# Optimization experiments

Hardware: AMD Instinct MI355X
Metric: run time of the kernel (lower is better)

## Reference

```python
import jax, jax.numpy as jnp
import numpy as np

NUM_EDGE = 5
NUM_CHANNELS = 2
NUM_NODES = 2048
W_IN = 256
W_OUT = 128
NUM_CLASS = 16
NUM_LAYERS = 2


def gtconv(A, w):
    """Softmax-weighted mix of edge-type adjacencies.
    A: [E, N, N], w: [E, C] -> [C, N, N].
    Equivalent to concatenating COO edge lists scaled by filter[j, i] and
    summing duplicates (what the scipy round-trip does implicitly)."""
    f = jax.nn.softmax(w, axis=0)  # softmax over edge types (dim=0)
    return jnp.einsum('enm,ec->cnm', A, f)


def degree_normalize(H):
    """GTN.normalization: deg = scatter_add over col, value *= deg[col]^-1 (col scaling).
    H: [C, N, N]; deg over rows (axis=1) gives per-column in-degree."""
    deg = H.sum(axis=1)  # [C, N]
    dinv = jnp.where(deg > 0, 1.0 / jnp.where(deg > 0, deg, 1.0), 0.0)
    return H * dinv[:, None, :]


def setup_inputs() -> dict:
    key = jax.random.key(0)
    ks = jax.random.split(key, 8)
    A = jax.random.uniform(ks[0], (NUM_EDGE, NUM_NODES, NUM_NODES), dtype=jnp.float32)
    h = jax.random.normal(ks[1], (NUM_NODES, W_IN), dtype=jnp.float32)
    # GTConv weights: init std=0.01 as in reset_parameters
    w1 = jax.random.normal(ks[2], (NUM_EDGE, NUM_CHANNELS), dtype=jnp.float32) * 0.01
    w2 = jax.random.normal(ks[3], (NUM_EDGE, NUM_CHANNELS), dtype=jnp.float32) * 0.01
    w_layers = jax.random.normal(ks[4], (NUM_LAYERS - 1, NUM_EDGE, NUM_CHANNELS), dtype=jnp.float32) * 0.01
    gcn_w = jax.random.normal(ks[5], (W_IN, W_OUT), dtype=jnp.float32) * (1.0 / np.sqrt(W_IN))
    gcn_b = jnp.zeros((W_OUT,), dtype=jnp.float32)
    lin1_w = jax.random.normal(ks[6], (W_OUT * NUM_CHANNELS, W_OUT), dtype=jnp.float32) * (1.0 / np.sqrt(W_OUT * NUM_CHANNELS))
    lin1_b = jnp.zeros((W_OUT,), dtype=jnp.float32)
    lin2_w = jax.random.normal(ks[7], (W_OUT, NUM_CLASS), dtype=jnp.float32) * (1.0 / np.sqrt(W_OUT))
    lin2_b = jnp.zeros((NUM_CLASS,), dtype=jnp.float32)
    return {"A": A, "h": h, "w1": w1, "w2": w2, "w_layers": w_layers,
            "gcn_w": gcn_w, "gcn_b": gcn_b, "lin1_w": lin1_w, "lin1_b": lin1_b,
            "lin2_w": lin2_w, "lin2_b": lin2_b}


def reference(A, h, w1, w2, w_layers, gcn_w, gcn_b, lin1_w, lin1_b, lin2_w, lin2_b):
    # Layer 0 (first=True): H[c] = conv1(A)[c] @ conv2(A)[c], then degree norm.
    H = jnp.einsum('cnk,ckm->cnm', gtconv(A, w1), gtconv(A, w2))
    H = degree_normalize(H)
    # Layers 1..L-1 (first=False): H[c] = H[c] @ conv(A)[c], then degree norm.
    for i in range(w_layers.shape[0]):
        B = gtconv(A, w_layers[i])
        H = jnp.einsum('cnk,ckm->cnm', H, B)
        H = degree_normalize(H)
    # Shared GCN per channel (DGL GraphConv, norm='both'): weight first (w_in > w_out),
    # src out-degree^-1/2 scaling, aggregate along edges src->dst, dst in-degree^-1/2.
    hw = h @ gcn_w                                   # [N, w_out]
    dout = jnp.clip(H.sum(axis=2), 1.0, None) ** -0.5  # [C, N] src norm
    din = jnp.clip(H.sum(axis=1), 1.0, None) ** -0.5   # [C, N] dst norm
    agg = jnp.einsum('cnm,cnd->cmd', H, dout[:, :, None] * hw[None])  # dst m gathers from src n
    X = jax.nn.relu(agg * din[:, :, None] + gcn_b)   # [C, N, w_out]
    # Concatenate channels along feature dim (channel-major, matching th.cat order)
    X = jnp.transpose(X, (1, 0, 2)).reshape(H.shape[1], -1)  # [N, C*w_out]
    X = jax.nn.relu(X @ lin1_w + lin1_b)
    return X @ lin2_w + lin2_b
```

## Files before the change

### kernel.cpp

```cpp
#include <hip/hip_runtime.h>

typedef unsigned short u16;
typedef __attribute__((ext_vector_type(4))) float f32x4;
typedef __attribute__((ext_vector_type(8))) __bf16 bf16x8;
typedef __attribute__((ext_vector_type(8))) unsigned short us8;

#define NN (2048ull*2048ull)

__device__ __forceinline__ u16 f2b(float x){
  union { float f; unsigned u; } v; v.f = x;
  unsigned r = v.u + 0x7FFFu + ((v.u >> 16) & 1u);
  return (u16)(r >> 16);
}
__device__ __forceinline__ float b2f(u16 x){
  union { unsigned u; float f; } v; v.u = ((unsigned)x) << 16; return v.f;
}

__global__ __launch_bounds__(256)
void k_mix(const float* __restrict__ A,
           const float* __restrict__ w1, const float* __restrict__ w2,
           const float* __restrict__ wl,
           u16* __restrict__ A1T, u16* __restrict__ A2T, u16* __restrict__ BT,
           float* __restrict__ sA1, float* __restrict__ deg2){
  __shared__ u16 lt[2][64][72];
  const int t = threadIdx.x;
  const int mq = t & 15, nr = t >> 4;
  const int n0 = blockIdx.y * 64, m0 = blockIdx.x * 64;
  float f[3][2][5];
  #pragma unroll
  for (int s=0;s<3;s++){
    const float* w = (s==0) ? w1 : (s==1) ? w2 : wl;
    #pragma unroll
    for (int c=0;c<2;c++){
      float m = -1e30f;
      #pragma unroll
      for (int e=0;e<5;e++) m = fmaxf(m, w[e*2+c]);
      float sum = 0.f;
      #pragma unroll
      for (int e=0;e<5;e++){ f[s][c][e] = __expf(w[e*2+c]-m); sum += f[s][c][e]; }
      float inv = 1.f/sum;
      #pragma unroll
      for (int e=0;e<5;e++) f[s][c][e] *= inv;
    }
  }

  ushort4 reg[6][4];
  #pragma unroll
  for (int rr=0; rr<4; ++rr){
    const int nl = nr*4 + rr;
    const size_t off = (size_t)(n0+nl)*2048 + m0 + mq*4;
    float4 a0 = *(const float4*)&A[off];
    float4 a1 = *(const float4*)&A[NN + off];
    float4 a2 = *(const float4*)&A[2*NN + off];
    float4 a3 = *(const float4*)&A[3*NN + off];
    float4 a4 = *(const float4*)&A[4*NN + off];
    float ax[4][5] = {{a0.x,a1.x,a2.x,a3.x,a4.x},
                      {a0.y,a1.y,a2.y,a3.y,a4.y},
                      {a0.z,a1.z,a2.z,a3.z,a4.z},
                      {a0.w,a1.w,a2.w,a3.w,a4.w}};
    #pragma unroll
    for (int c=0;c<2;c++){
      #pragma unroll
      for (int j=0;j<4;j++){
        float s1=0.f,s2=0.f,s3=0.f;
        #pragma unroll
        for (int e=0;e<5;e++){
          s1 += ax[j][e]*f[0][c][e];
          s2 += ax[j][e]*f[1][c][e];
          s3 += ax[j][e]*f[2][c][e];
        }
        ((u16*)&reg[0+c][rr])[j] = f2b(s1);
        ((u16*)&reg[2+c][rr])[j] = f2b(s2);
        ((u16*)&reg[4+c][rr])[j] = f2b(s3);
      }
    }
  }

  const int nq = t & 15, mr = t >> 4;
  for (int s=0; s<3; ++s){
    if (s) __syncthreads();
    #pragma unroll
    for (int c=0;c<2;c++){
      #pragma unroll
      for (int j=0;j<4;j++){
        ushort4 o;
        o.x = ((const u16*)&reg[s*2+c][0])[j];
        o.y = ((const u16*)&reg[s*2+c][1])[j];
        o.z = ((const u16*)&reg[s*2+c][2])[j];
        o.w = ((const u16*)&reg[s*2+c][3])[j];
        *(ushort4*)&lt[c][mq*4+j][nr*4] = o;
      }
    }
    __syncthreads();
    u16* __restrict__ dst = (s==0) ? A1T : (s==1) ? A2T : BT;
    #pragma unroll
    for (int c=0;c<2;c++){
      #pragma unroll
      for (int rr=0;rr<4;rr++){
        const int ml = mr*4 + rr;
        ushort4 o = *(const ushort4*)&lt[c][ml][nq*4];
        *(ushort4*)&dst[(size_t)c*NN + (size_t)(m0+ml)*2048 + n0 + nq*4] = o;
        if (s != 1){
          float part = b2f(o.x)+b2f(o.y)+b2f(o.z)+b2f(o.w);
          part += __shfl_xor(part, 1); part += __shfl_xor(part, 2);
          part += __shfl_xor(part, 4); part += __shfl_xor(part, 8);
          if (nq == 0){
            float* tgt = (s==0) ? sA1 : deg2;
            atomicAdd(&tgt[c*2048 + m0 + ml], part);
          }
        }
      }
    }
  }
}

__global__ __launch_bounds__(256)
void k_deg1(const u16* __restrict__ A2T, const float* __restrict__ sA1,
            float* __restrict__ deg1){
  const int g = blockIdx.x*4 + (threadIdx.x >> 6);
  const int lane = threadIdx.x & 63;
  const int c = g >> 11, j = g & 2047;
  const u16* __restrict__ row = A2T + (size_t)c*NN + (size_t)j*2048;
  const float* __restrict__ sv = sA1 + c*2048;
  float s = 0.f;
  #pragma unroll
  for (int it=0; it<4; ++it){
    const int k = it*512 + lane*8;
    us8 v = *(const us8*)&row[k];
    const float4 f0 = *(const float4*)&sv[k];
    const float4 f1 = *(const float4*)&sv[k+4];
    s += b2f(v[0])*f0.x + b2f(v[1])*f0.y + b2f(v[2])*f0.z + b2f(v[3])*f0.w
       + b2f(v[4])*f1.x + b2f(v[5])*f1.y + b2f(v[6])*f1.z + b2f(v[7])*f1.w;
  }
  s += __shfl_xor(s, 1);  s += __shfl_xor(s, 2);  s += __shfl_xor(s, 4);
  s += __shfl_xor(s, 8);  s += __shfl_xor(s, 16); s += __shfl_xor(s, 32);
  if (lane == 0) deg1[c*2048 + j] = s;
}

template<int MODE>
__global__ __launch_bounds__(256)
void k_wsum(const u16* __restrict__ MT, const float* __restrict__ va,
            const float* __restrict__ vb, float* __restrict__ outv){
  __shared__ float w[128];
  const int t = threadIdx.x;
  const int n = blockIdx.x * 256 + t;
  const int m0 = blockIdx.y * 128;
  const int c = blockIdx.z;
  if (t < 128){
    const int m = c*2048 + m0 + t;
    float x;
    if (MODE == 0){ float d = va[m]; x = d > 0.f ? 1.f/d : 0.f; }
    else if (MODE == 1){ float d = va[m]; x = (d > 0.f ? 1.f/d : 0.f) * vb[m]; }
    else { x = va[m]; }
    w[t] = x;
  }
  __syncthreads();
  const u16* __restrict__ p = MT + (size_t)c*NN + (size_t)m0*2048 + n;
  float s = 0.f;
  #pragma unroll 4
  for (int m=0;m<128;m++)
    s += b2f(p[(size_t)m*2048]) * w[m];
  atomicAdd(&outv[c*2048 + n], s);
}

__global__ __launch_bounds__(256)
void k_hw(const float* __restrict__ h, const float* __restrict__ W, float* __restrict__ hw){
  __shared__ float lh[16][256];
  int t = threadIdx.x;
  int n0 = blockIdx.x * 16;
  for (int idx = t; idx < 16*256; idx += 256)
    lh[idx >> 8][idx & 255] = h[(size_t)(n0 + (idx>>8))*256 + (idx&255)];
  __syncthreads();
  int d = t & 127, half = t >> 7;
  float acc[8];
  #pragma unroll
  for (int nn=0;nn<8;nn++) acc[nn] = 0.f;
  for (int k=0;k<256;k++){
    float wv = W[(size_t)k*128 + d];
    #pragma unroll
    for (int nn=0;nn<8;nn++) acc[nn] += lh[half*8+nn][k]*wv;
  }
  #pragma unroll
  for (int nn=0;nn<8;nn++) hw[(size_t)(n0 + half*8 + nn)*128 + d] = acc[nn];
}

__global__ void k_pt(const float* __restrict__ hw, const float* __restrict__ rowsum,
                     u16* __restrict__ PT){
  int t = threadIdx.x;
  int n = blockIdx.x * 64 + (t & 63);
  int c = blockIdx.y;
  float dv = rsqrtf(fmaxf(rowsum[c*2048 + n], 1.0f));
  for (int d = t >> 6; d < 128; d += 4)
    PT[((size_t)c*128 + d)*2048 + n] = f2b(dv * hw[(size_t)n*128 + d]);
}

__global__ __launch_bounds__(256, 2)
void k_gemm3(const u16* __restrict__ A, const u16* __restrict__ Bt, float* __restrict__ Cp){
  __shared__ u16 lA[128*64];
  __shared__ u16 lB[128*64];
  const int tid = threadIdx.x;
  const int bm = blockIdx.x, bk = blockIdx.y, cc = blockIdx.z;
  const u16* __restrict__ Ab = A + (size_t)cc*NN + (size_t)(bm*128)*2048 + bk*256;
  const u16* __restrict__ Bb = Bt + (size_t)cc*(128*2048) + bk*256;
  float* __restrict__ Cb = Cp + ((size_t)bk*2 + cc)*2048*128 + (size_t)(bm*128)*128;
  const int wid = tid >> 6, lane = tid & 63;
  const int wr = wid >> 1, wc = wid & 1;
  const int fl = lane & 15, fk = (lane >> 4) << 3;
  const int srow = (wid << 3) + (lane >> 3);
  const int scol = (lane & 7) << 3;

  f32x4 acc[4][4];
  const f32x4 zero = {0.f,0.f,0.f,0.f};
  #pragma unroll
  for (int i=0;i<4;i++)
    #pragma unroll
    for (int jj=0;jj<4;jj++) acc[i][jj] = zero;

  for (int k0 = 0; k0 < 256; k0 += 64){
    #pragma unroll
    for (int it = 0; it < 4; ++it){
      int r = it*32 + srow;
      __builtin_amdgcn_global_load_lds(
        (const __attribute__((address_space(1))) void*)(Ab + (size_t)r*2048 + k0 + scol),
        (__attribute__((address_space(3))) void*)(&lA[(it*32 + (wid<<3))*64]), 16, 0, 0);
      __builtin_amdgcn_global_load_lds(
        (const __attribute__((address_space(1))) void*)(Bb + (size_t)r*2048 + k0 + scol),
        (__attribute__((address_space(3))) void*)(&lB[(it*32 + (wid<<3))*64]), 16, 0, 0);
    }
    __syncthreads();
    #pragma unroll
    for (int ks = 0; ks < 2; ++ks){
      bf16x8 af[4], bfr[4];
      #pragma unroll
      for (int mi=0;mi<4;mi++)
        af[mi] = *reinterpret_cast<const bf16x8*>(&lA[(wr*64 + mi*16 + fl)*64 + ks*32 + fk]);
      #pragma unroll
      for (int ni=0;ni<4;ni++)
        bfr[ni] = *reinterpret_cast<const bf16x8*>(&lB[(wc*64 + ni*16 + fl)*64 + ks*32 + fk]);
      #pragma unroll
      for (int mi=0;mi<4;mi++)
        #pragma unroll
        for (int ni=0;ni<4;ni++)
          acc[mi][ni] = __builtin_amdgcn_mfma_f32_16x16x32_bf16(af[mi], bfr[ni], acc[mi][ni], 0, 0, 0);
    }
    __syncthreads();
  }
  const int rbase = (lane >> 4) << 2;
  #pragma unroll
  for (int mi=0;mi<4;mi++)
    #pragma unroll
    for (int ni=0;ni<4;ni++)
      #pragma unroll
      for (int r=0;r<4;r++)
        Cb[(size_t)(wr*64 + mi*16 + rbase + r)*128 + wc*64 + ni*16 + fl] = acc[mi][ni][r];
}

template<bool SCALE>
__global__ __launch_bounds__(256)
void k_redt(const float* __restrict__ aggp, const float* __restrict__ deg1,
            u16* __restrict__ QT){
  __shared__ u16 lq[128][36];
  const int t = threadIdx.x;
  const int m0 = blockIdx.x * 32, c = blockIdx.y;
  const int d4 = (t & 31) * 4, mr = t >> 5;
  #pragma unroll
  for (int p4=0; p4<4; ++p4){
    const int m = m0 + p4*8 + mr;
    float4 s = {0.f,0.f,0.f,0.f};
    #pragma unroll
    for (int p=0;p<8;p++){
      const float4 v = *(const float4*)&aggp[(((size_t)p*2 + c)*2048 + m)*128 + d4];
      s.x += v.x; s.y += v.y; s.z += v.z; s.w += v.w;
    }
    if (SCALE){
      float dg = deg1[c*2048 + m];
      float di = dg > 0.f ? 1.f/dg : 0.f;
      s.x *= di; s.y *= di; s.z *= di; s.w *= di;
    }
    const int ml = p4*8 + mr;
    lq[d4+0][ml] = f2b(s.x); lq[d4+1][ml] = f2b(s.y);
    lq[d4+2][ml] = f2b(s.z); lq[d4+3][ml] = f2b(s.w);
  }
  __syncthreads();
  const int d = t >> 1, half = t & 1;
  u16* __restrict__ dst = QT + ((size_t)c*128 + d)*2048 + m0 + half*16;
  #pragma unroll
  for (int q=0;q<4;q++){
    ushort4 o;
    o.x = lq[d][half*16 + q*4 + 0];
    o.y = lq[d][half*16 + q*4 + 1];
    o.z = lq[d][half*16 + q*4 + 2];
    o.w = lq[d][half*16 + q*4 + 3];
    *(ushort4*)&dst[q*4] = o;
  }
}

__global__ __launch_bounds__(256)
void k_head(const float* __restrict__ aggp, const float* __restrict__ deg2,
            const float* __restrict__ gb,
            const float* __restrict__ W1, const float* __restrict__ b1,
            const float* __restrict__ W2, const float* __restrict__ b2,
            float* __restrict__ out){
  __shared__ float lx[16][256];
  __shared__ float lt[16][132];
  int t = threadIdx.x;
  int n0 = blockIdx.x * 16;
  for (int idx = t; idx < 1024; idx += 256){
    int row = idx >> 6;
    int q = idx & 63;
    int c = q >> 5, d4 = (q & 31) * 4;
    float dg = deg2[c*2048 + n0 + row];
    float di = dg > 0.f ? 1.f/dg : 0.f;
    float4 s = {0.f,0.f,0.f,0.f};
    #pragma unroll
    for (int p=0;p<8;p++){
      const float4 v = *(const float4*)&aggp[(((size_t)p*2 + c)*2048 + n0 + row)*128 + d4];
      s.x += v.x; s.y += v.y; s.z += v.z; s.w += v.w;
    }
    const float4 bv = *(const float4*)&gb[d4];
    s.x = fmaxf(s.x*di + bv.x, 0.f); s.y = fmaxf(s.y*di + bv.y, 0.f);
    s.z = fmaxf(s.z*di + bv.z, 0.f); s.w = fmaxf(s.w*di + bv.w, 0.f);
    *(float4*)&lx[row][c*128 + d4] = s;
  }
  __syncthreads();
  int d = t & 127, half = t >> 7;
  float acc[8];
  #pragma unroll
  for (int nn=0;nn<8;nn++) acc[nn] = 0.f;
  for (int k=0;k<256;k++){
    float wv = W1[(size_t)k*128 + d];
    #pragma unroll
    for (int nn=0;nn<8;nn++) acc[nn] += lx[half*8+nn][k]*wv;
  }
  float bb = b1[d];
  #pragma unroll
  for (int nn=0;nn<8;nn++){
    float v = acc[nn] + bb;
    lt[half*8+nn][d] = v > 0.f ? v : 0.f;
  }
  __syncthreads();
  {
    int row = t >> 4, q = t & 15;
    float s = b2[q];
    for (int dd=0; dd<128; dd++) s += lt[row][dd] * W2[(size_t)dd*16 + q];
    out[(size_t)(n0+row)*16 + q] = s;
  }
}

extern "C" void kernel_launch(void* const* d_in, const int* in_sizes, int n_in,
                              void* d_out, int out_size, void* d_ws, size_t ws_size,
                              hipStream_t stream){
  const float* A   = (const float*)d_in[0];
  const float* h   = (const float*)d_in[1];
  const float* w1  = (const float*)d_in[2];
  const float* w2  = (const float*)d_in[3];
  const float* wl  = (const float*)d_in[4];
  const float* gw  = (const float*)d_in[5];
  const float* gb  = (const float*)d_in[6];
  const float* l1w = (const float*)d_in[7];
  const float* l1b = (const float*)d_in[8];
  const float* l2w = (const float*)d_in[9];
  const float* l2b = (const float*)d_in[10];
  float* out = (float*)d_out;
  char* ws = (char*)d_ws;

  const size_t SZ = 2*NN*2;
  u16*  A1T  = (u16*)(ws);
  u16*  A2T  = (u16*)(ws + 1*SZ);
  u16*  BT   = (u16*)(ws + 2*SZ);
  float* aggp= (float*)(ws + 3*SZ);
  char* tail = ws + 4*SZ;
  float* hw    = (float*)tail;
  u16*  PT     = (u16*)(tail + 1048576);
  u16*  Q1T    = (u16*)(tail + 2*1048576);
  u16*  Q2T    = (u16*)(tail + 3*1048576);
  float* sA1   = (float*)(tail + 4*1048576);
  float* deg1  = sA1 + 4096;
  float* deg2  = deg1 + 4096;
  float* v1    = deg2 + 4096;
  float* v3    = v1 + 4096;
  float* rowsum= v3 + 4096;

  const size_t TOTAL = 4*SZ + 4*1048576 + 6*4096*4;
  if (ws_size < TOTAL){ hipMemsetAsync(d_out, 0, (size_t)out_size*4, stream); return; }

  hipMemsetAsync(sA1, 0, 6*4096*4, stream);

  k_mix<<<dim3(32,32), 256, 0, stream>>>(A, w1, w2, wl, A1T, A2T, BT, sA1, deg2);
  k_deg1<<<1024, 256, 0, stream>>>(A2T, sA1, deg1);
  k_wsum<0><<<dim3(8,16,2), 256, 0, stream>>>(BT, deg2, deg2, v1);
  k_wsum<1><<<dim3(8,16,2), 256, 0, stream>>>(A2T, deg1, v1, v3);
  k_wsum<2><<<dim3(8,16,2), 256, 0, stream>>>(A1T, v3, v3, rowsum);
  k_hw<<<128, 256, 0, stream>>>(h, gw, hw);
  k_pt<<<dim3(32,2), 256, 0, stream>>>(hw, rowsum, PT);
  k_gemm3<<<dim3(16,8,2), 256, 0, stream>>>(A1T, PT, aggp);
  k_redt<false><<<dim3(64,2), 256, 0, stream>>>(aggp, deg1, Q1T);
  k_gemm3<<<dim3(16,8,2), 256, 0, stream>>>(A2T, Q1T, aggp);
  k_redt<true><<<dim3(64,2), 256, 0, stream>>>(aggp, deg1, Q2T);
  k_gemm3<<<dim3(16,8,2), 256, 0, stream>>>(BT, Q2T, aggp);
  k_head<<<128, 256, 0, stream>>>(aggp, deg2, gb, l1w, l1b, l2w, l2b, out);
}
```

Before: 164.1 us.

## Fuse hw/pt kernels, atomic split-K accumulation, smaller tiles for small kernels

```diff
diff --git a/kernel.cpp b/kernel.cpp
--- a/kernel.cpp
+++ b/kernel.cpp
@@ -22,7 +22,7 @@
            const float* __restrict__ wl,
            u16* __restrict__ A1T, u16* __restrict__ A2T, u16* __restrict__ BT,
            float* __restrict__ sA1, float* __restrict__ deg2){
-  __shared__ u16 lt[2][64][72];
+  __shared__ u16 lt[2][64][68];
   const int t = threadIdx.x;
   const int mq = t & 15, nr = t >> 4;
   const int n0 = blockIdx.y * 64, m0 = blockIdx.x * 64;
@@ -141,12 +141,12 @@
 __global__ __launch_bounds__(256)
 void k_wsum(const u16* __restrict__ MT, const float* __restrict__ va,
             const float* __restrict__ vb, float* __restrict__ outv){
-  __shared__ float w[128];
+  __shared__ float w[64];
   const int t = threadIdx.x;
   const int n = blockIdx.x * 256 + t;
-  const int m0 = blockIdx.y * 128;
+  const int m0 = blockIdx.y * 64;
   const int c = blockIdx.z;
-  if (t < 128){
+  if (t < 64){
     const int m = c*2048 + m0 + t;
     float x;
     if (MODE == 0){ float d = va[m]; x = d > 0.f ? 1.f/d : 0.f; }
@@ -158,51 +158,51 @@
   const u16* __restrict__ p = MT + (size_t)c*NN + (size_t)m0*2048 + n;
   float s = 0.f;
   #pragma unroll 4
-  for (int m=0;m<128;m++)
+  for (int m=0;m<64;m++)
     s += b2f(p[(size_t)m*2048]) * w[m];
   atomicAdd(&outv[c*2048 + n], s);
 }
 
 __global__ __launch_bounds__(256)
-void k_hw(const float* __restrict__ h, const float* __restrict__ W, float* __restrict__ hw){
-  __shared__ float lh[16][256];
+void k_hwpt(const float* __restrict__ h, const float* __restrict__ W,
+            const float* __restrict__ rowsum, u16* __restrict__ PT){
+  __shared__ float lh[8][256];
   int t = threadIdx.x;
-  int n0 = blockIdx.x * 16;
-  for (int idx = t; idx < 16*256; idx += 256)
+  int n0 = blockIdx.x * 8;
+  for (int idx = t; idx < 8*256; idx += 256)
     lh[idx >> 8][idx & 255] = h[(size_t)(n0 + (idx>>8))*256 + (idx&255)];
   __syncthreads();
   int d = t & 127, half = t >> 7;
-  float acc[8];
-  #pragma unroll
-  for (int nn=0;nn<8;nn++) acc[nn] = 0.f;
+  float acc[4];
+  #pragma unroll
+  for (int nn=0;nn<4;nn++) acc[nn] = 0.f;
   for (int k=0;k<256;k++){
     float wv = W[(size_t)k*128 + d];
     #pragma unroll
-    for (int nn=0;nn<8;nn++) acc[nn] += lh[half*8+nn][k]*wv;
-  }
-  #pragma unroll
-  for (int nn=0;nn<8;nn++) hw[(size_t)(n0 + half*8 + nn)*128 + d] = acc[nn];
-}
-
-__global__ void k_pt(const float* __restrict__ hw, const float* __restrict__ rowsum,
-                     u16* __restrict__ PT){
-  int t = threadIdx.x;
-  int n = blockIdx.x * 64 + (t & 63);
-  int c = blockIdx.y;
-  float dv = rsqrtf(fmaxf(rowsum[c*2048 + n], 1.0f));
-  for (int d = t >> 6; d < 128; d += 4)
-    PT[((size_t)c*128 + d)*2048 + n] = f2b(dv * hw[(size_t)n*128 + d]);
+    for (int nn=0;nn<4;nn++) acc[nn] += lh[half*4+nn][k]*wv;
+  }
+  #pragma unroll
+  for (int c=0;c<2;c++){
+    ushort4 o;
+    #pragma unroll
+    for (int nn=0;nn<4;nn++){
+      int n = n0 + half*4 + nn;
+      float dv = rsqrtf(fmaxf(rowsum[c*2048 + n], 1.0f));
+      ((u16*)&o)[nn] = f2b(dv * acc[nn]);
+    }
+    *(ushort4*)&PT[((size_t)c*128 + d)*2048 + n0 + half*4] = o;
+  }
 }
 
 __global__ __launch_bounds__(256, 2)
-void k_gemm3(const u16* __restrict__ A, const u16* __restrict__ Bt, float* __restrict__ Cp){
+void k_gemm3(const u16* __restrict__ A, const u16* __restrict__ Bt, float* __restrict__ Agg){
   __shared__ u16 lA[128*64];
   __shared__ u16 lB[128*64];
   const int tid = threadIdx.x;
   const int bm = blockIdx.x, bk = blockIdx.y, cc = blockIdx.z;
   const u16* __restrict__ Ab = A + (size_t)cc*NN + (size_t)(bm*128)*2048 + bk*256;
   const u16* __restrict__ Bb = Bt + (size_t)cc*(128*2048) + bk*256;
-  float* __restrict__ Cb = Cp + ((size_t)bk*2 + cc)*2048*128 + (size_t)(bm*128)*128;
+  float* __restrict__ Cb = Agg + (size_t)cc*2048*128 + (size_t)(bm*128)*128;
   const int wid = tid >> 6, lane = tid & 63;
   const int wr = wid >> 1, wc = wid & 1;
   const int fl = lane & 15, fk = (lane >> 4) << 3;
@@ -252,13 +252,14 @@
     for (int ni=0;ni<4;ni++)
       #pragma unroll
       for (int r=0;r<4;r++)
-        Cb[(size_t)(wr*64 + mi*16 + rbase + r)*128 + wc*64 + ni*16 + fl] = acc[mi][ni][r];
+        atomicAdd(&Cb[(size_t)(wr*64 + mi*16 + rbase + r)*128 + wc*64 + ni*16 + fl],
+                  acc[mi][ni][r]);
 }
 
 template<bool SCALE>
 __global__ __launch_bounds__(256)
-void k_redt(const float* __restrict__ aggp, const float* __restrict__ deg1,
-            u16* __restrict__ QT){
+void k_qt(const float* __restrict__ Agg, const float* __restrict__ deg1,
+          u16* __restrict__ QT){
   __shared__ u16 lq[128][36];
   const int t = threadIdx.x;
   const int m0 = blockIdx.x * 32, c = blockIdx.y;
@@ -266,12 +267,7 @@
   #pragma unroll
   for (int p4=0; p4<4; ++p4){
     const int m = m0 + p4*8 + mr;
-    float4 s = {0.f,0.f,0.f,0.f};
-    #pragma unroll
-    for (int p=0;p<8;p++){
-      const float4 v = *(const float4*)&aggp[(((size_t)p*2 + c)*2048 + m)*128 + d4];
-      s.x += v.x; s.y += v.y; s.z += v.z; s.w += v.w;
-    }
+    float4 s = *(const float4*)&Agg[((size_t)c*2048 + m)*128 + d4];
     if (SCALE){
       float dg = deg1[c*2048 + m];
       float di = dg > 0.f ? 1.f/dg : 0.f;
@@ -296,27 +292,22 @@
 }
 
 __global__ __launch_bounds__(256)
-void k_head(const float* __restrict__ aggp, const float* __restrict__ deg2,
+void k_head(const float* __restrict__ agg3, const float* __restrict__ deg2,
             const float* __restrict__ gb,
             const float* __restrict__ W1, const float* __restrict__ b1,
             const float* __restrict__ W2, const float* __restrict__ b2,
             float* __restrict__ out){
-  __shared__ float lx[16][256];
-  __shared__ float lt[16][132];
+  __shared__ float lx[8][256];
+  __shared__ float lt[8][132];
   int t = threadIdx.x;
-  int n0 = blockIdx.x * 16;
-  for (int idx = t; idx < 1024; idx += 256){
+  int n0 = blockIdx.x * 8;
+  for (int idx = t; idx < 512; idx += 256){
     int row = idx >> 6;
     int q = idx & 63;
     int c = q >> 5, d4 = (q & 31) * 4;
     float dg = deg2[c*2048 + n0 + row];
     float di = dg > 0.f ? 1.f/dg : 0.f;
-    float4 s = {0.f,0.f,0.f,0.f};
-    #pragma unroll
-    for (int p=0;p<8;p++){
-      const float4 v = *(const float4*)&aggp[(((size_t)p*2 + c)*2048 + n0 + row)*128 + d4];
-      s.x += v.x; s.y += v.y; s.z += v.z; s.w += v.w;
-    }
+    float4 s = *(const float4*)&agg3[((size_t)c*2048 + n0 + row)*128 + d4];
     const float4 bv = *(const float4*)&gb[d4];
     s.x = fmaxf(s.x*di + bv.x, 0.f); s.y = fmaxf(s.y*di + bv.y, 0.f);
     s.z = fmaxf(s.z*di + bv.z, 0.f); s.w = fmaxf(s.w*di + bv.w, 0.f);
@@ -324,22 +315,22 @@
   }
   __syncthreads();
   int d = t & 127, half = t >> 7;
-  float acc[8];
-  #pragma unroll
-  for (int nn=0;nn<8;nn++) acc[nn] = 0.f;
+  float acc[4];
+  #pragma unroll
+  for (int nn=0;nn<4;nn++) acc[nn] = 0.f;
   for (int k=0;k<256;k++){
     float wv = W1[(size_t)k*128 + d];
     #pragma unroll
-    for (int nn=0;nn<8;nn++) acc[nn] += lx[half*8+nn][k]*wv;
+    for (int nn=0;nn<4;nn++) acc[nn] += lx[half*4+nn][k]*wv;
   }
   float bb = b1[d];
   #pragma unroll
-  for (int nn=0;nn<8;nn++){
+  for (int nn=0;nn<4;nn++){
     float v = acc[nn] + bb;
-    lt[half*8+nn][d] = v > 0.f ? v : 0.f;
-  }
-  __syncthreads();
-  {
+    lt[half*4+nn][d] = v > 0.f ? v : 0.f;
+  }
+  __syncthreads();
+  if (t < 128){
     int row = t >> 4, q = t & 15;
     float s = b2[q];
     for (int dd=0; dd<128; dd++) s += lt[row][dd] * W2[(size_t)dd*16 + q];
@@ -365,38 +356,40 @@
   char* ws = (char*)d_ws;
 
   const size_t SZ = 2*NN*2;
+  const size_t AGG = (size_t)2*2048*128*4;
   u16*  A1T  = (u16*)(ws);
   u16*  A2T  = (u16*)(ws + 1*SZ);
   u16*  BT   = (u16*)(ws + 2*SZ);
-  float* aggp= (float*)(ws + 3*SZ);
-  char* tail = ws + 4*SZ;
-  float* hw    = (float*)tail;
-  u16*  PT     = (u16*)(tail + 1048576);
-  u16*  Q1T    = (u16*)(tail + 2*1048576);
-  u16*  Q2T    = (u16*)(tail + 3*1048576);
-  float* sA1   = (float*)(tail + 4*1048576);
+  char* tail = ws + 3*SZ;
+  u16*  PT     = (u16*)tail;
+  u16*  Q1T    = (u16*)(tail + 1048576);
+  u16*  Q2T    = (u16*)(tail + 2*1048576);
+  float* sA1   = (float*)(tail + 3*1048576);
   float* deg1  = sA1 + 4096;
   float* deg2  = deg1 + 4096;
   float* v1    = deg2 + 4096;
   float* v3    = v1 + 4096;
   float* rowsum= v3 + 4096;
-
-  const size_t TOTAL = 4*SZ + 4*1048576 + 6*4096*4;
+  float* agg1  = rowsum + 4096;
+  float* agg2  = agg1 + 2*2048*128;
+  float* agg3  = agg2 + 2*2048*128;
+  const size_t ZBYTES = 6*4096*4 + 3*AGG;
+
+  const size_t TOTAL = 3*SZ + 3*1048576 + ZBYTES;
   if (ws_size < TOTAL){ hipMemsetAsync(d_out, 0, (size_t)out_size*4, stream); return; }
 
-  hipMemsetAsync(sA1, 0, 6*4096*4, stream);
+  hipMemsetAsync(sA1, 0, ZBYTES, stream);
 
   k_mix<<<dim3(32,32), 256, 0, stream>>>(A, w1, w2, wl, A1T, A2T, BT, sA1, deg2);
   k_deg1<<<1024, 256, 0, stream>>>(A2T, sA1, deg1);
-  k_wsum<0><<<dim3(8,16,2), 256, 0, stream>>>(BT, deg2, deg2, v1);
-  k_wsum<1><<<dim3(8,16,2), 256, 0, stream>>>(A2T, deg1, v1, v3);
-  k_wsum<2><<<dim3(8,16,2), 256, 0, stream>>>(A1T, v3, v3, rowsum);
-  k_hw<<<128, 256, 0, stream>>>(h, gw, hw);
-  k_pt<<<dim3(32,2), 256, 0, stream>>>(hw, rowsum, PT);
-  k_gemm3<<<dim3(16,8,2), 256, 0, stream>>>(A1T, PT, aggp);
-  k_redt<false><<<dim3(64,2), 256, 0, stream>>>(aggp, deg1, Q1T);
-  k_gemm3<<<dim3(16,8,2), 256, 0, stream>>>(A2T, Q1T, aggp);
-  k_redt<true><<<dim3(64,2), 256, 0, stream>>>(aggp, deg1, Q2T);
-  k_gemm3<<<dim3(16,8,2), 256, 0, stream>>>(BT, Q2T, aggp);
-  k_head<<<128, 256, 0, stream>>>(aggp, deg2, gb, l1w, l1b, l2w, l2b, out);
-}
+  k_wsum<0><<<dim3(8,32,2), 256, 0, stream>>>(BT, deg2, deg2, v1);
+  k_wsum<1><<<dim3(8,32,2), 256, 0, stream>>>(A2T, deg1, v1, v3);
+  k_wsum<2><<<dim3(8,32,2), 256, 0, stream>>>(A1T, v3, v3, rowsum);
+  k_hwpt<<<256, 256, 0, stream>>>(h, gw, rowsum, PT);
+  k_gemm3<<<dim3(16,8,2), 256, 0, stream>>>(A1T, PT, agg1);
+  k_qt<false><<<dim3(64,2), 256, 0, stream>>>(agg1, deg1, Q1T);
+  k_gemm3<<<dim3(16,8,2), 256, 0, stream>>>(A2T, Q1T, agg2);
+  k_qt<true><<<dim3(64,2), 256, 0, stream>>>(agg2, deg1, Q2T);
+  k_gemm3<<<dim3(16,8,2), 256, 0, stream>>>(BT, Q2T, agg3);
+  k_head<<<256, 256, 0, stream>>>(agg3, deg2, gb, l1w, l1b, l2w, l2b, out);
+}
```

After: 160.0 us. -2.5%, faster.
